# Performance work log

Measured on AMD Instinct MI355X. Metric: run time of the kernel, lower is better.

Reference implementation:

```python
import jax, jax.numpy as jnp
import numpy as np

B, N, F_IN, DEG = 8, 4096, 8, 8
E = B * N * DEG
MAX_RADIUS, NUM_BASIS, HIDDEN = 3.0, 10, 64
MUL0, MUL1 = 32, 16  # irreps_potential = '32x0e + 16x1o'
W_NUMEL = F_IN * (MUL0 + MUL1)  # 384


def setup_inputs() -> dict:
    key = jax.random.key(0)
    k1, k2, k3, k4, k5, k6 = jax.random.split(key, 6)
    node_features = jax.random.normal(k1, (B, N, F_IN), jnp.float32)
    pos = 4.0 * jax.random.uniform(k2, (B, N, 3), dtype=jnp.float32)  # box so many pairs fall inside max_radius
    # static-shape stand-in for radius_graph: DEG random neighbors per node, within each graph, no self loops
    src = jax.random.randint(k3, (B, N * DEG), 0, N)
    off = jax.random.randint(k4, (B, N * DEG), 1, N)
    dst = (src + off) % N
    boff = (jnp.arange(B) * N)[:, None]
    edge_src = (src + boff).reshape(-1).astype(jnp.int32)
    edge_dst = (dst + boff).reshape(-1).astype(jnp.int32)
    W1 = jax.random.normal(k5, (NUM_BASIS, HIDDEN), jnp.float32)
    W2 = jax.random.normal(k6, (HIDDEN, W_NUMEL), jnp.float32)
    return {"node_features": node_features, "pos": pos, "edge_src": edge_src,
            "edge_dst": edge_dst, "W1": W1, "W2": W2}


def _forward(node_features, pos, edge_src, edge_dst, W1, W2):
    pos_flat = pos.reshape(-1, 3)            # [B*N, 3]
    x_flat = node_features.reshape(-1, F_IN)  # [B*N, F_IN]
    edge_vec = pos_flat[edge_src] - pos_flat[edge_dst]  # [E,3]
    r = jnp.sqrt(jnp.sum(edge_vec * edge_vec, axis=1) + 1e-18)  # [E]

    # soft_one_hot_linspace(r, 0, R, num_basis, basis='smooth_finite', cutoff=True) * sqrt(num_basis)
    values = jnp.linspace(0.0, MAX_RADIUS, NUM_BASIS + 2)[1:-1]
    step = values[1] - values[0]
    d = (r[:, None] - values[None, :]) / step
    inside = jnp.abs(d) < 1.0
    y = jnp.where(inside, jnp.maximum(1.0 - d * d, 1e-7), 1.0)
    emb = jnp.where(inside, 1.14136 * jnp.exp(2.0) * jnp.exp(-1.0 / y), 0.0)
    emb = emb * (NUM_BASIS ** 0.5)           # [E, num_basis]

    # soft_unit_step(10 * (1 - r/R))
    t = 10.0 * (1.0 - r / MAX_RADIUS)
    w_cut = jnp.where(t > 0.0, jnp.exp(-1.0 / jnp.where(t > 0.0, t, 1.0)), 0.0)

    # spherical harmonics lmax=2, normalize=True, 'component' normalization
    u = edge_vec / r[:, None]
    ux, uy, uz = u[:, 0], u[:, 1], u[:, 2]
    sh1 = jnp.sqrt(3.0) * u                  # l=1 (component norm); sh0 == 1
    c15 = np.sqrt(15.0)
    sh2 = jnp.stack([c15 * ux * uy, c15 * uy * uz, 0.5 * np.sqrt(5.0) * (3 * uz * uz - 1.0),
                     c15 * ux * uz, 0.5 * c15 * (ux * ux - uy * uy)], axis=1)
    del sh2  # 2e couples 0e input only to 2e, which is absent from '32x0e+16x1o' -> no path

    # FullyConnectedNet([num_basis, hidden, weight_numel], silu) -> per-edge TP weights
    h = jax.nn.silu(emb @ (W1 / np.sqrt(NUM_BASIS)))
    w = h @ (W2 / np.sqrt(HIDDEN))           # [E, 384]
    wA = w[:, : F_IN * MUL0].reshape(-1, F_IN, MUL0)
    wB = w[:, F_IN * MUL0:].reshape(-1, F_IN, MUL1)

    # FullyConnectedTensorProduct (uvw), shared_weights=False, path norm 1/sqrt(fan_in)
    x_src = x_flat[edge_src]                 # gather [E, F_IN]
    inv = 1.0 / np.sqrt(F_IN)
    out0 = jnp.einsum('eu,euw->ew', x_src, wA) * inv            # 0e x 0e -> 32x0e
    out1 = jnp.einsum('eu,ei,euw->ewi', x_src, sh1, wB) * inv   # 0e x 1o -> 16x1o
    potential = jnp.concatenate([out0, out1.reshape(-1, 3 * MUL1)], axis=1)  # [E, 80]

    # scatter-add to destination nodes
    nodes = jax.ops.segment_sum(w_cut[:, None] * potential, edge_dst, num_segments=B * N)
    psi = nodes[:, :3].reshape(B, N, 3)
    curl = jnp.stack([psi[..., 2] - psi[..., 1],
                      psi[..., 0] - psi[..., 2],
                      psi[..., 1] - psi[..., 0]], axis=-1)       # [B, N, 3]
    return curl


def reference(node_features, pos, edge_src, edge_dst, W1, W2):
    return _forward(node_features, pos, edge_src, edge_dst, W1, W2)
```

## Files before the change

### kernel.cpp

```cpp
#include <hip/hip_runtime.h>


#define THREADS 256
#define TROW 32

__global__ __launch_bounds__(THREADS) void se3_build_table(
    const float* __restrict__ W1,
    const float* __restrict__ W2,
    float* __restrict__ T,
    int R)
{
    __shared__ float sW1[10 * 65];
    for (int t = threadIdx.x; t < 640; t += THREADS) {
        int j = t >> 6, k = t & 63;
        sW1[j * 65 + k] = W1[t];
    }
    __syncthreads();

    int g = blockIdx.x * THREADS + threadIdx.x;
    if (g >= R * 24) return;
    int i = g / 24;
    int j = g - i * 24;
    int u = j / 3, c = j - u * 3;

    float r = 3.0f * (float)i / (float)(R - 1);

    const float C0 = 8.43357306907549f;
    float q  = r * (11.0f / 3.0f);
    int   jf = (int)q;
    float da = q - (float)jf;
    float db = da - 1.0f;
    float ya = fmaxf(1.0f - da * da, 1e-7f);
    float yb = fmaxf(1.0f - db * db, 1e-7f);
    int ja = jf - 1, jb = jf;
    float ea = (ja >= 0) ? C0 * __expf(-1.0f / ya) : 0.0f;
    float eb = (jb <= 9) ? C0 * __expf(-1.0f / yb) : 0.0f;
    int jac = ja < 0 ? 0 : ja;
    int jbc = jb > 9 ? 9 : jb;
    const float* w1a = sW1 + jac * 65;
    const float* w1b = sW1 + jbc * 65;
    const float* w2  = W2 + u * 32 + c;

    float acc = 0.0f;
#pragma unroll 8
    for (int k = 0; k < 64; ++k) {
        float pre = ea * w1a[k] + eb * w1b[k];
        float h   = pre / (1.0f + __expf(-pre));
        acc += h * w2[k * 384];
    }
    T[i * TROW + j] = acc;
}

__global__ __launch_bounds__(THREADS) void se3_edge_kernel(
    const float* __restrict__ x,
    const float* __restrict__ pos,
    const int*   __restrict__ esrc,
    const int*   __restrict__ edst,
    const float* __restrict__ T,
    float*       __restrict__ outbuf,
    int E, int ncopies, int outN, float rscale, int imax)
{
    int e = blockIdx.x * THREADS + threadIdx.x;
    if (e >= E) return;

    int s = esrc[e];
    int d = edst[e];

    float ex = pos[3 * s + 0] - pos[3 * d + 0];
    float ey = pos[3 * s + 1] - pos[3 * d + 1];
    float ez = pos[3 * s + 2] - pos[3 * d + 2];
    float r  = sqrtf(ex * ex + ey * ey + ez * ez + 1e-18f);

    float t10 = 10.0f - (10.0f / 3.0f) * r;
    if (t10 <= 0.0f) return;
    float wcut = __expf(-1.0f / t10);

    float tq = r * rscale;
    int   i  = (int)tq;
    if (i > imax) i = imax;
    float f  = tq - (float)i;

    const float4* T0 = reinterpret_cast<const float4*>(T + (size_t)i * TROW);
    float tv0[24], tv1[24];
#pragma unroll
    for (int q4 = 0; q4 < 6; ++q4) {
        float4 v0 = T0[q4];
        float4 v1 = T0[q4 + (TROW / 4)];
        tv0[4*q4+0] = v0.x; tv0[4*q4+1] = v0.y; tv0[4*q4+2] = v0.z; tv0[4*q4+3] = v0.w;
        tv1[4*q4+0] = v1.x; tv1[4*q4+1] = v1.y; tv1[4*q4+2] = v1.z; tv1[4*q4+3] = v1.w;
    }

    const float4* xf = reinterpret_cast<const float4*>(x + 8 * (size_t)s);
    float4 xA = xf[0];
    float4 xB = xf[1];
    float xs[8] = {xA.x, xA.y, xA.z, xA.w, xB.x, xB.y, xB.z, xB.w};

    float p0 = 0.0f, p1 = 0.0f, p2 = 0.0f;
#pragma unroll
    for (int u = 0; u < 8; ++u) {
        float xu = xs[u];
        int b = 3 * u;
        p0 = fmaf(xu, fmaf(f, tv1[b+0] - tv0[b+0], tv0[b+0]), p0);
        p1 = fmaf(xu, fmaf(f, tv1[b+1] - tv0[b+1], tv0[b+1]), p1);
        p2 = fmaf(xu, fmaf(f, tv1[b+2] - tv0[b+2], tv0[b+2]), p2);
    }

    float sc = wcut * 0.04419417382415922f;
    p0 *= sc; p1 *= sc; p2 *= sc;

    float* ob = outbuf + (size_t)(blockIdx.x % ncopies) * outN + 3 * d;
    atomicAdd(ob + 0, p2 - p1);
    atomicAdd(ob + 1, p0 - p2);
    atomicAdd(ob + 2, p1 - p0);
}

__global__ __launch_bounds__(THREADS) void se3_reduce_kernel(
    const float* __restrict__ ws, float* __restrict__ out,
    int outN4, int ncopies)
{
    int idx = blockIdx.x * THREADS + threadIdx.x;
    if (idx >= outN4) return;
    const float4* w = reinterpret_cast<const float4*>(ws);
    float4 acc = w[idx];
    for (int c = 1; c < ncopies; ++c) {
        float4 v = w[(size_t)c * outN4 + idx];
        acc.x += v.x; acc.y += v.y; acc.z += v.z; acc.w += v.w;
    }
    reinterpret_cast<float4*>(out)[idx] = acc;
}

extern "C" void kernel_launch(void* const* d_in, const int* in_sizes, int n_in,
                              void* d_out, int out_size, void* d_ws, size_t ws_size,
                              hipStream_t stream) {
    const float* x    = (const float*)d_in[0];
    const float* pos  = (const float*)d_in[1];
    const int*   esrc = (const int*)d_in[2];
    const int*   edst = (const int*)d_in[3];
    const float* W1   = (const float*)d_in[4];
    const float* W2   = (const float*)d_in[5];
    float* out = (float*)d_out;

    int E    = in_sizes[2];
    int outN = out_size;

    int R = 2048;
    while (R > 64 && (size_t)R * TROW * sizeof(float) > ws_size) R >>= 1;
    size_t tableFloats = (size_t)R * TROW;
    size_t tableBytes  = tableFloats * sizeof(float);

    int ncopies = 0;
    if (ws_size >= tableBytes) {
        size_t rem = ws_size - tableBytes;
        ncopies = (int)(rem / ((size_t)outN * sizeof(float)));
        if (ncopies > 8) ncopies = 8;
    }

    float* T = (float*)d_ws;
    float rscale = (float)(R - 1) / 3.0f;
    int   imax   = R - 2;

    int buildBlocks = (R * 24 + THREADS - 1) / THREADS;
    se3_build_table<<<buildBlocks, THREADS, 0, stream>>>(W1, W2, T, R);

    int edgeBlocks = (E + THREADS - 1) / THREADS;
    if (ncopies >= 2) {
        float* copies = T + tableFloats;
        hipMemsetAsync(copies, 0, (size_t)ncopies * outN * sizeof(float), stream);
        se3_edge_kernel<<<edgeBlocks, THREADS, 0, stream>>>(
            x, pos, esrc, edst, T, copies, E, ncopies, outN, rscale, imax);
        int outN4 = outN / 4;
        se3_reduce_kernel<<<(outN4 + THREADS - 1) / THREADS, THREADS, 0, stream>>>(
            copies, out, outN4, ncopies);
    } else {
        hipMemsetAsync(out, 0, (size_t)outN * sizeof(float), stream);
        se3_edge_kernel<<<edgeBlocks, THREADS, 0, stream>>>(
            x, pos, esrc, edst, T, out, E, 1, outN, rscale, imax);
    }
}
```

Baseline: 106.6 us.

## Store interpolation table in fp16 with interleaved neighbor rows and folded cutoff

The radial lookup table now holds fp16 values, and each row stores entry i next to entry i+1, so an edge reads a single 96-byte row instead of two float rows. The smooth cutoff factor and the normalization constant are folded into the table, which removes the per-edge exp. The table size is now fixed at 2048 rows regardless of workspace size. This reduces gather traffic and per-edge arithmetic at the cost of fp16 precision in the table, and linear interpolation of the cutoff-weighted function may add some approximation error.

```diff
diff --git a/kernel.cpp b/kernel.cpp
--- a/kernel.cpp
+++ b/kernel.cpp
@@ -1,14 +1,15 @@
 #include <hip/hip_runtime.h>
+#include <hip/hip_fp16.h>
 
 
 #define THREADS 256
-#define TROW 32
+#define RTAB 2048
+#define ROWH 64
 
 __global__ __launch_bounds__(THREADS) void se3_build_table(
     const float* __restrict__ W1,
     const float* __restrict__ W2,
-    float* __restrict__ T,
-    int R)
+    __half* __restrict__ T)
 {
     __shared__ float sW1[10 * 65];
     for (int t = threadIdx.x; t < 640; t += THREADS) {
@@ -18,37 +19,45 @@
     __syncthreads();
 
     int g = blockIdx.x * THREADS + threadIdx.x;
-    if (g >= R * 24) return;
+    if (g >= RTAB * 24) return;
     int i = g / 24;
     int j = g - i * 24;
     int u = j / 3, c = j - u * 3;
 
-    float r = 3.0f * (float)i / (float)(R - 1);
+    float r = 3.0f * (float)i / (float)(RTAB - 1);
 
-    const float C0 = 8.43357306907549f;
-    float q  = r * (11.0f / 3.0f);
-    int   jf = (int)q;
-    float da = q - (float)jf;
-    float db = da - 1.0f;
-    float ya = fmaxf(1.0f - da * da, 1e-7f);
-    float yb = fmaxf(1.0f - db * db, 1e-7f);
-    int ja = jf - 1, jb = jf;
-    float ea = (ja >= 0) ? C0 * __expf(-1.0f / ya) : 0.0f;
-    float eb = (jb <= 9) ? C0 * __expf(-1.0f / yb) : 0.0f;
-    int jac = ja < 0 ? 0 : ja;
-    int jbc = jb > 9 ? 9 : jb;
-    const float* w1a = sW1 + jac * 65;
-    const float* w1b = sW1 + jbc * 65;
-    const float* w2  = W2 + u * 32 + c;
+    float psi = 0.0f;
+    float t10 = 10.0f - (10.0f / 3.0f) * r;
+    if (t10 > 0.0f) {
+        const float C0 = 8.43357306907549f;
+        float q  = r * (11.0f / 3.0f);
+        int   jf = (int)q;
+        float da = q - (float)jf;
+        float db = da - 1.0f;
+        float ya = fmaxf(1.0f - da * da, 1e-7f);
+        float yb = fmaxf(1.0f - db * db, 1e-7f);
+        int ja = jf - 1, jb = jf;
+        float ea = (ja >= 0) ? C0 * __expf(-1.0f / ya) : 0.0f;
+        float eb = (jb <= 9) ? C0 * __expf(-1.0f / yb) : 0.0f;
+        int jac = ja < 0 ? 0 : ja;
+        int jbc = jb > 9 ? 9 : jb;
+        const float* w1a = sW1 + jac * 65;
+        const float* w1b = sW1 + jbc * 65;
+        const float* w2  = W2 + u * 32 + c;
 
-    float acc = 0.0f;
+        float acc = 0.0f;
 #pragma unroll 8
-    for (int k = 0; k < 64; ++k) {
-        float pre = ea * w1a[k] + eb * w1b[k];
-        float h   = pre / (1.0f + __expf(-pre));
-        acc += h * w2[k * 384];
+        for (int k = 0; k < 64; ++k) {
+            float pre = ea * w1a[k] + eb * w1b[k];
+            float h   = pre * __builtin_amdgcn_rcpf(1.0f + __expf(-pre));
+            acc += h * w2[k * 384];
+        }
+        psi = acc * __expf(-1.0f / t10) * 0.04419417382415922f;
     }
-    T[i * TROW + j] = acc;
+
+    __half hv = __float2half(psi);
+    T[(size_t)i * ROWH + 2 * j] = hv;
+    if (i > 0) T[(size_t)(i - 1) * ROWH + 2 * j + 1] = hv;
 }
 
 __global__ __launch_bounds__(THREADS) void se3_edge_kernel(
@@ -56,9 +65,9 @@
     const float* __restrict__ pos,
     const int*   __restrict__ esrc,
     const int*   __restrict__ edst,
-    const float* __restrict__ T,
+    const __half* __restrict__ T,
     float*       __restrict__ outbuf,
-    int E, int ncopies, int outN, float rscale, int imax)
+    int E, int ncopies, int outN)
 {
     int e = blockIdx.x * THREADS + threadIdx.x;
     if (e >= E) return;
@@ -71,47 +80,38 @@
     float ez = pos[3 * s + 2] - pos[3 * d + 2];
     float r  = sqrtf(ex * ex + ey * ey + ez * ez + 1e-18f);
 
-    float t10 = 10.0f - (10.0f / 3.0f) * r;
-    if (t10 <= 0.0f) return;
-    float wcut = __expf(-1.0f / t10);
+    if (r >= 3.0f) return;
 
-    float tq = r * rscale;
+    float tq = r * ((float)(RTAB - 1) / 3.0f);
     int   i  = (int)tq;
-    if (i > imax) i = imax;
+    if (i > RTAB - 2) i = RTAB - 2;
     float f  = tq - (float)i;
 
-    const float4* T0 = reinterpret_cast<const float4*>(T + (size_t)i * TROW);
-    float tv0[24], tv1[24];
-#pragma unroll
-    for (int q4 = 0; q4 < 6; ++q4) {
-        float4 v0 = T0[q4];
-        float4 v1 = T0[q4 + (TROW / 4)];
-        tv0[4*q4+0] = v0.x; tv0[4*q4+1] = v0.y; tv0[4*q4+2] = v0.z; tv0[4*q4+3] = v0.w;
-        tv1[4*q4+0] = v1.x; tv1[4*q4+1] = v1.y; tv1[4*q4+2] = v1.z; tv1[4*q4+3] = v1.w;
-    }
-
-    const float4* xf = reinterpret_cast<const float4*>(x + 8 * (size_t)s);
+    const float4* rowp = reinterpret_cast<const float4*>(T + (size_t)i * ROWH);
+    const float4* xf   = reinterpret_cast<const float4*>(x + 8 * (size_t)s);
     float4 xA = xf[0];
     float4 xB = xf[1];
     float xs[8] = {xA.x, xA.y, xA.z, xA.w, xB.x, xB.y, xB.z, xB.w};
 
-    float p0 = 0.0f, p1 = 0.0f, p2 = 0.0f;
+    float p[3] = {0.0f, 0.0f, 0.0f};
 #pragma unroll
-    for (int u = 0; u < 8; ++u) {
-        float xu = xs[u];
-        int b = 3 * u;
-        p0 = fmaf(xu, fmaf(f, tv1[b+0] - tv0[b+0], tv0[b+0]), p0);
-        p1 = fmaf(xu, fmaf(f, tv1[b+1] - tv0[b+1], tv0[b+1]), p1);
-        p2 = fmaf(xu, fmaf(f, tv1[b+2] - tv0[b+2], tv0[b+2]), p2);
+    for (int qi = 0; qi < 6; ++qi) {
+        float4 v = rowp[qi];
+        const __half2* h2 = reinterpret_cast<const __half2*>(&v);
+#pragma unroll
+        for (int m = 0; m < 4; ++m) {
+            int j = 4 * qi + m;
+            int u = j / 3, c = j - 3 * u;
+            float2 ab = __half22float2(h2[m]);
+            float val = fmaf(f, ab.y - ab.x, ab.x);
+            p[c] = fmaf(xs[u], val, p[c]);
+        }
     }
 
-    float sc = wcut * 0.04419417382415922f;
-    p0 *= sc; p1 *= sc; p2 *= sc;
-
     float* ob = outbuf + (size_t)(blockIdx.x % ncopies) * outN + 3 * d;
-    atomicAdd(ob + 0, p2 - p1);
-    atomicAdd(ob + 1, p0 - p2);
-    atomicAdd(ob + 2, p1 - p0);
+    atomicAdd(ob + 0, p[2] - p[1]);
+    atomicAdd(ob + 1, p[0] - p[2]);
+    atomicAdd(ob + 2, p[1] - p[0]);
 }
 
 __global__ __launch_bounds__(THREADS) void se3_reduce_kernel(
@@ -143,37 +143,33 @@
     int E    = in_sizes[2];
     int outN = out_size;
 
-    int R = 2048;
-    while (R > 64 && (size_t)R * TROW * sizeof(float) > ws_size) R >>= 1;
-    size_t tableFloats = (size_t)R * TROW;
-    size_t tableBytes  = tableFloats * sizeof(float);
+    size_t tableBytes = (size_t)RTAB * ROWH * sizeof(__half);
+    __half* T = (__half*)d_ws;
 
-    int ncopies = 0;
-    if (ws_size >= tableBytes) {
+    int ncopies = 1;
+    if (ws_size > tableBytes) {
         size_t rem = ws_size - tableBytes;
-        ncopies = (int)(rem / ((size_t)outN * sizeof(float)));
-        if (ncopies > 8) ncopies = 8;
+        int nc = (int)(rem / ((size_t)outN * sizeof(float)));
+        if (nc > 8) nc = 8;
+        if (nc < 1) nc = 1;
+        ncopies = nc;
     }
 
-    float* T = (float*)d_ws;
-    float rscale = (float)(R - 1) / 3.0f;
-    int   imax   = R - 2;
-
-    int buildBlocks = (R * 24 + THREADS - 1) / THREADS;
-    se3_build_table<<<buildBlocks, THREADS, 0, stream>>>(W1, W2, T, R);
+    int buildBlocks = (RTAB * 24 + THREADS - 1) / THREADS;
+    se3_build_table<<<buildBlocks, THREADS, 0, stream>>>(W1, W2, T);
 
     int edgeBlocks = (E + THREADS - 1) / THREADS;
     if (ncopies >= 2) {
-        float* copies = T + tableFloats;
+        float* copies = (float*)((char*)d_ws + tableBytes);
         hipMemsetAsync(copies, 0, (size_t)ncopies * outN * sizeof(float), stream);
         se3_edge_kernel<<<edgeBlocks, THREADS, 0, stream>>>(
-            x, pos, esrc, edst, T, copies, E, ncopies, outN, rscale, imax);
+            x, pos, esrc, edst, T, copies, E, ncopies, outN);
         int outN4 = outN / 4;
         se3_reduce_kernel<<<(outN4 + THREADS - 1) / THREADS, THREADS, 0, stream>>>(
             copies, out, outN4, ncopies);
     } else {
         hipMemsetAsync(out, 0, (size_t)outN * sizeof(float), stream);
         se3_edge_kernel<<<edgeBlocks, THREADS, 0, stream>>>(
-            x, pos, esrc, edst, T, out, E, 1, outN, rscale, imax);
+            x, pos, esrc, edst, T, out, E, 1, outN);
     }
 }
```

Measured after the change: 105.6 us. Within noise of the previous version (-0.9%).
